# Optimization experiments

Measured on AMD Instinct MI355X. Metric: run time of the kernel, lower is better.

The kernel has to match this reference:

```python
import jax, jax.numpy as jnp
import numpy as np

B, OBS, H, A = 262144, 64, 64, 16
ACTION_LOW, ACTION_HIGH = -1.0, 1.0


def setup_inputs() -> dict:
    key = jax.random.key(0)
    ks = jax.random.split(key, 11)
    s = 0.05
    return {
        "obs": jax.random.normal(ks[0], (B, OBS), dtype=jnp.float32),
        "h0": jax.random.normal(ks[1], (1, B, H), dtype=jnp.float32),
        "c0": jax.random.normal(ks[2], (1, B, H), dtype=jnp.float32),
        "W_in": jax.random.normal(ks[3], (H, OBS), dtype=jnp.float32) * s,
        "b_in": jax.random.normal(ks[4], (H,), dtype=jnp.float32) * s,
        "W_ih": jax.random.normal(ks[5], (4 * H, H), dtype=jnp.float32) * s,
        "W_hh": jax.random.normal(ks[6], (4 * H, H), dtype=jnp.float32) * s,
        "b_ih": jax.random.normal(ks[7], (4 * H,), dtype=jnp.float32) * s,
        "b_hh": jax.random.normal(ks[8], (4 * H,), dtype=jnp.float32) * s,
        "W_out": jax.random.normal(ks[9], (A, H), dtype=jnp.float32) * s,
        "b_out": jax.random.normal(ks[10], (A,), dtype=jnp.float32) * s,
    }


def reference(obs, h0, c0, W_in, b_in, W_ih, W_hh, b_ih, b_hh, W_out, b_out):
    # input projection: [B, H]
    x = obs @ W_in.T + b_in
    h, c = h0[0], c0[0]  # [B, H] each (num_layers=1, seq_len=1)
    # single-step LSTM cell, PyTorch gate order (i, f, g, o)
    gates = x @ W_ih.T + b_ih + h @ W_hh.T + b_hh  # [B, 4H]
    i, f, g, o = jnp.split(gates, 4, axis=-1)
    i = jax.nn.sigmoid(i)
    f = jax.nn.sigmoid(f)
    g = jnp.tanh(g)
    o = jax.nn.sigmoid(o)
    c_new = f * c + i * g
    h_new = o * jnp.tanh(c_new)
    a = jnp.tanh(h_new @ W_out.T + b_out)  # [B, A]
    action = ACTION_LOW + (a + 1.0) * 0.5 * (ACTION_HIGH - ACTION_LOW)
    return action, h_new[None], c_new[None]
```

## Files before the change

### kernel.cpp

```cpp
#include <hip/hip_runtime.h>
#include <hip/hip_bf16.h>

#define BT 262144
#define BLOCK 512
#define NBLOCKS 512
#define NIT 4

typedef __attribute__((ext_vector_type(8))) short short8;
typedef __attribute__((ext_vector_type(4))) float f32x4;
typedef __attribute__((ext_vector_type(4))) unsigned short u16x4;

__device__ __forceinline__ unsigned short f2bf(float f) {
  union { __hip_bfloat16 b; unsigned short u; } v;
  v.b = __float2bfloat16(f);
  return v.u;
}
__device__ __forceinline__ float frcp(float x) { return __builtin_amdgcn_rcpf(x); }
__device__ __forceinline__ float sigm(float x) { return frcp(1.0f + __expf(-x)); }
__device__ __forceinline__ float tanh_(float x) {
  float e = __expf(-2.0f * x);
  return (1.0f - e) * frcp(1.0f + e);
}

__global__ void prep_kernel(const float* __restrict__ W_in, const float* __restrict__ b_in,
                            const float* __restrict__ W_ih, const float* __restrict__ W_hh,
                            const float* __restrict__ b_ih, const float* __restrict__ b_hh,
                            const float* __restrict__ W_out,
                            unsigned short* __restrict__ wsW, float* __restrict__ ws_beff) {
  int id = blockIdx.x * blockDim.x + threadIdx.x;
  if (id < 16384) {
    int j = id & 7, l = (id >> 3) & 63, a = (id >> 9) & 15, ks = id >> 13;
    int n = (a >> 2) * 64 + 4 * (l & 15) + (a & 3);
    int k = ks * 32 + (l >> 4) * 8 + j;
    float s = 0.f;
    #pragma unroll 8
    for (int h = 0; h < 64; ++h) s = fmaf(W_ih[n * 64 + h], W_in[h * 64 + k], s);
    wsW[id] = f2bf(s);
  } else if (id < 32768) {
    int e = id - 16384;
    int j = e & 7, l = (e >> 3) & 63, a = (e >> 9) & 15, ks = (e >> 13) & 1;
    int n = (a >> 2) * 64 + 4 * (l & 15) + (a & 3);
    int k = ks * 32 + (l >> 4) * 8 + j;
    wsW[id] = f2bf(W_hh[n * 64 + k]);
  } else if (id < 33792) {
    int e = id - 32768;
    int j = e & 7, l = (e >> 3) & 63, ks = e >> 9;
    int n = l & 15;
    int k = ks * 32 + (l >> 4) * 8 + j;
    wsW[id] = f2bf(W_out[n * 64 + k]);
  } else if (id < 34048) {
    int n = id - 33792;
    float s = b_ih[n] + b_hh[n];
    #pragma unroll 8
    for (int h = 0; h < 64; ++h) s = fmaf(W_ih[n * 64 + h], b_in[h], s);
    ws_beff[n] = s;
  }
}

__device__ __forceinline__ short8 pack8(float4 lo, float4 hi) {
  short8 r;
  r[0] = (short)f2bf(lo.x); r[1] = (short)f2bf(lo.y);
  r[2] = (short)f2bf(lo.z); r[3] = (short)f2bf(lo.w);
  r[4] = (short)f2bf(hi.x); r[5] = (short)f2bf(hi.y);
  r[6] = (short)f2bf(hi.z); r[7] = (short)f2bf(hi.w);
  return r;
}

__global__ __launch_bounds__(BLOCK, 2) void lstm_main(
    const float* __restrict__ obs, const float* __restrict__ h0,
    const float* __restrict__ c0, const float* __restrict__ b_out,
    const unsigned short* __restrict__ wsW, const float* __restrict__ ws_beff,
    float* __restrict__ out) {
  __shared__ __attribute__((aligned(16))) unsigned char sbuf[65536];
  __shared__ __attribute__((aligned(16))) unsigned short hbuf[8][1024];
  unsigned short* sw = (unsigned short*)sbuf;

  const int tid = threadIdx.x;
  const int wv = tid >> 6;
  const int lane = tid & 63;
  const int l16 = lane & 15;
  const int q = lane >> 4;

  for (int i = tid; i < 4096; i += BLOCK)
    ((uint4*)sbuf)[i] = ((const uint4*)wsW)[i];
  __syncthreads();

  const float boA = b_out[l16];

  const short8* wEv = (const short8*)sw;
  const short8* wHv = (const short8*)(sw + 16384);
  const short8* wOg = (const short8*)(wsW + 32768);
  unsigned short* hb = &hbuf[wv][0];

  float* out_act = out;
  float* out_h = out + (size_t)BT * 16;
  float* out_c = out + (size_t)BT * 80;

  float4 ro[2][4], rh[2][4];
  f32x4 cold[2][4];

  auto tile_rowbase = [&](int it) -> size_t {
    return ((size_t)(it * NBLOCKS + blockIdx.x)) * 128 + (size_t)wv * 16;
  };
  auto load_oh = [&](int it, int buf) {
    size_t rowbase = tile_rowbase(it);
    const float* po = obs + (rowbase + l16) * 64 + q * 8;
    const float* ph = h0 + (rowbase + l16) * 64 + q * 8;
    ro[buf][0] = *(const float4*)(po);
    ro[buf][1] = *(const float4*)(po + 4);
    ro[buf][2] = *(const float4*)(po + 32);
    ro[buf][3] = *(const float4*)(po + 36);
    rh[buf][0] = *(const float4*)(ph);
    rh[buf][1] = *(const float4*)(ph + 4);
    rh[buf][2] = *(const float4*)(ph + 32);
    rh[buf][3] = *(const float4*)(ph + 36);
  };
  auto load_c0 = [&](int it, int buf) {
    size_t rowbase = tile_rowbase(it);
    #pragma unroll
    for (int r = 0; r < 4; ++r)
      cold[buf][r] = *(const f32x4*)(c0 + (rowbase + (size_t)(4 * q + r)) * 64 + 4 * l16);
  };

  load_oh(0, 0);
  load_c0(0, 0);
  #pragma unroll
  for (int it = 0; it < NIT; ++it) {
    const int cur = it & 1;
    const size_t rowbase = tile_rowbase(it);

    if (it + 1 < NIT) {
      load_oh(it + 1, cur ^ 1);
      load_c0(it + 1, cur ^ 1);
    }

    f32x4 bias_g[4];
    #pragma unroll
    for (int g = 0; g < 4; ++g)
      bias_g[g] = *(const f32x4*)(ws_beff + g * 64 + 4 * l16);

    short8 aObs[2], aH[2];
    aObs[0] = pack8(ro[cur][0], ro[cur][1]);
    aObs[1] = pack8(ro[cur][2], ro[cur][3]);
    aH[0]   = pack8(rh[cur][0], rh[cur][1]);
    aH[1]   = pack8(rh[cur][2], rh[cur][3]);

    f32x4 acc[16];
    #pragma unroll
    for (int a = 0; a < 16; ++a) {
      float b = bias_g[a >> 2][a & 3];
      acc[a] = (f32x4){b, b, b, b};
    }

    #pragma unroll
    for (int ks = 0; ks < 2; ++ks) {
      #pragma unroll
      for (int a = 0; a < 16; ++a) {
        acc[a] = __builtin_amdgcn_mfma_f32_16x16x32_bf16(aObs[ks], wEv[(ks * 16 + a) * 64 + lane], acc[a], 0, 0, 0);
        acc[a] = __builtin_amdgcn_mfma_f32_16x16x32_bf16(aH[ks],  wHv[(ks * 16 + a) * 64 + lane], acc[a], 0, 0, 0);
      }
    }

    #pragma unroll
    for (int r = 0; r < 4; ++r) {
      f32x4 c4, h4;
      u16x4 hb4;
      #pragma unroll
      for (int t = 0; t < 4; ++t) {
        float iv = sigm(acc[t][r]);
        float fv = sigm(acc[4 + t][r]);
        float gv = tanh_(acc[8 + t][r]);
        float ov = sigm(acc[12 + t][r]);
        float cnew = fmaf(fv, cold[cur][r][t], iv * gv);
        float hnew = ov * tanh_(cnew);
        c4[t] = cnew;
        h4[t] = hnew;
        hb4[t] = f2bf(hnew);
      }
      const int hrow = 4 * q + r;
      const size_t m = rowbase + (size_t)hrow;
      __builtin_nontemporal_store(c4, (f32x4*)(out_c + m * 64 + 4 * l16));
      __builtin_nontemporal_store(h4, (f32x4*)(out_h + m * 64 + 4 * l16));
      *(u16x4*)(hb + hrow * 64 + ((4 * l16) ^ ((hrow & 7) << 3))) = hb4;
    }

    f32x4 aA = (f32x4){boA, boA, boA, boA};
    short8 a0 = *(const short8*)(hb + l16 * 64 + ((0 * 32 + q * 8) ^ ((l16 & 7) << 3)));
    short8 a1 = *(const short8*)(hb + l16 * 64 + ((1 * 32 + q * 8) ^ ((l16 & 7) << 3)));
    aA = __builtin_amdgcn_mfma_f32_16x16x32_bf16(a0, wOg[lane], aA, 0, 0, 0);
    aA = __builtin_amdgcn_mfma_f32_16x16x32_bf16(a1, wOg[64 + lane], aA, 0, 0, 0);
    #pragma unroll
    for (int r = 0; r < 4; ++r) {
      size_t m = rowbase + (size_t)(4 * q + r);
      __builtin_nontemporal_store(tanh_(aA[r]), out_act + m * 16 + l16);
    }
  }
}

extern "C" void kernel_launch(void* const* d_in, const int* in_sizes, int n_in,
                              void* d_out, int out_size, void* d_ws, size_t ws_size,
                              hipStream_t stream) {
  const float* obs  = (const float*)d_in[0];
  const float* h0   = (const float*)d_in[1];
  const float* c0   = (const float*)d_in[2];
  const float* W_in = (const float*)d_in[3];
  const float* b_in = (const float*)d_in[4];
  const float* W_ih = (const float*)d_in[5];
  const float* W_hh = (const float*)d_in[6];
  const float* b_ih = (const float*)d_in[7];
  const float* b_hh = (const float*)d_in[8];
  const float* W_out = (const float*)d_in[9];
  const float* b_out = (const float*)d_in[10];

  unsigned short* wsW = (unsigned short*)d_ws;
  float* ws_beff = (float*)((char*)d_ws + 67584);

  prep_kernel<<<133, 256, 0, stream>>>(W_in, b_in, W_ih, W_hh, b_ih, b_hh, W_out, wsW, ws_beff);
  lstm_main<<<NBLOCKS, BLOCK, 0, stream>>>(obs, h0, c0, b_out, wsW, ws_beff, (float*)d_out);
}
```

Before: 68.22 us.

## Split output-head projection into a separate kernel reading h from global

Moves the action head (h_new @ W_out + tanh) out of the main LSTM kernel into a new act_kernel that re-reads h_new from the output buffer. This drops the per-wave LDS h buffer and the head MFMAs from the main kernel, freeing LDS and registers for occupancy, and h stores become regular cached stores so the second kernel may hit in cache. In exchange it adds a kernel launch and an extra 64 MB read of h from memory.

```diff
diff --git a/kernel.cpp b/kernel.cpp
--- a/kernel.cpp
+++ b/kernel.cpp
@@ -8,7 +8,6 @@
 
 typedef __attribute__((ext_vector_type(8))) short short8;
 typedef __attribute__((ext_vector_type(4))) float f32x4;
-typedef __attribute__((ext_vector_type(4))) unsigned short u16x4;
 
 __device__ __forceinline__ unsigned short f2bf(float f) {
   union { __hip_bfloat16 b; unsigned short u; } v;
@@ -68,11 +67,10 @@
 
 __global__ __launch_bounds__(BLOCK, 2) void lstm_main(
     const float* __restrict__ obs, const float* __restrict__ h0,
-    const float* __restrict__ c0, const float* __restrict__ b_out,
+    const float* __restrict__ c0,
     const unsigned short* __restrict__ wsW, const float* __restrict__ ws_beff,
     float* __restrict__ out) {
   __shared__ __attribute__((aligned(16))) unsigned char sbuf[65536];
-  __shared__ __attribute__((aligned(16))) unsigned short hbuf[8][1024];
   unsigned short* sw = (unsigned short*)sbuf;
 
   const int tid = threadIdx.x;
@@ -85,14 +83,9 @@
     ((uint4*)sbuf)[i] = ((const uint4*)wsW)[i];
   __syncthreads();
 
-  const float boA = b_out[l16];
-
   const short8* wEv = (const short8*)sw;
   const short8* wHv = (const short8*)(sw + 16384);
-  const short8* wOg = (const short8*)(wsW + 32768);
-  unsigned short* hb = &hbuf[wv][0];
-
-  float* out_act = out;
+
   float* out_h = out + (size_t)BT * 16;
   float* out_c = out + (size_t)BT * 80;
 
@@ -164,7 +157,6 @@
     #pragma unroll
     for (int r = 0; r < 4; ++r) {
       f32x4 c4, h4;
-      u16x4 hb4;
       #pragma unroll
       for (int t = 0; t < 4; ++t) {
         float iv = sigm(acc[t][r]);
@@ -175,25 +167,43 @@
         float hnew = ov * tanh_(cnew);
         c4[t] = cnew;
         h4[t] = hnew;
-        hb4[t] = f2bf(hnew);
       }
       const int hrow = 4 * q + r;
       const size_t m = rowbase + (size_t)hrow;
       __builtin_nontemporal_store(c4, (f32x4*)(out_c + m * 64 + 4 * l16));
-      __builtin_nontemporal_store(h4, (f32x4*)(out_h + m * 64 + 4 * l16));
-      *(u16x4*)(hb + hrow * 64 + ((4 * l16) ^ ((hrow & 7) << 3))) = hb4;
-    }
-
-    f32x4 aA = (f32x4){boA, boA, boA, boA};
-    short8 a0 = *(const short8*)(hb + l16 * 64 + ((0 * 32 + q * 8) ^ ((l16 & 7) << 3)));
-    short8 a1 = *(const short8*)(hb + l16 * 64 + ((1 * 32 + q * 8) ^ ((l16 & 7) << 3)));
-    aA = __builtin_amdgcn_mfma_f32_16x16x32_bf16(a0, wOg[lane], aA, 0, 0, 0);
-    aA = __builtin_amdgcn_mfma_f32_16x16x32_bf16(a1, wOg[64 + lane], aA, 0, 0, 0);
-    #pragma unroll
-    for (int r = 0; r < 4; ++r) {
-      size_t m = rowbase + (size_t)(4 * q + r);
-      __builtin_nontemporal_store(tanh_(aA[r]), out_act + m * 16 + l16);
-    }
+      *(f32x4*)(out_h + m * 64 + 4 * l16) = h4;
+    }
+  }
+}
+
+__global__ void act_kernel(const float* __restrict__ h,
+                           const float* __restrict__ b_out,
+                           const unsigned short* __restrict__ wsW,
+                           float* __restrict__ out_act) {
+  const int tid = threadIdx.x;
+  const int wv = tid >> 6;
+  const int lane = tid & 63;
+  const int l16 = lane & 15;
+  const int q = lane >> 4;
+  const size_t rowbase = ((size_t)blockIdx.x * 4 + (size_t)wv) * 16;
+
+  const float* ph = h + (rowbase + l16) * 64 + q * 8;
+  float4 h0v = *(const float4*)(ph);
+  float4 h1v = *(const float4*)(ph + 4);
+  float4 h2v = *(const float4*)(ph + 32);
+  float4 h3v = *(const float4*)(ph + 36);
+  short8 a0 = pack8(h0v, h1v);
+  short8 a1 = pack8(h2v, h3v);
+
+  const short8* wOg = (const short8*)(wsW + 32768);
+  const float bo = b_out[l16];
+  f32x4 aA = (f32x4){bo, bo, bo, bo};
+  aA = __builtin_amdgcn_mfma_f32_16x16x32_bf16(a0, wOg[lane], aA, 0, 0, 0);
+  aA = __builtin_amdgcn_mfma_f32_16x16x32_bf16(a1, wOg[64 + lane], aA, 0, 0, 0);
+  #pragma unroll
+  for (int r = 0; r < 4; ++r) {
+    size_t m = rowbase + (size_t)(4 * q + r);
+    __builtin_nontemporal_store(tanh_(aA[r]), out_act + m * 16 + l16);
   }
 }
 
@@ -215,6 +225,10 @@
   unsigned short* wsW = (unsigned short*)d_ws;
   float* ws_beff = (float*)((char*)d_ws + 67584);
 
+  float* out = (float*)d_out;
+  float* out_h = out + (size_t)BT * 16;
+
   prep_kernel<<<133, 256, 0, stream>>>(W_in, b_in, W_ih, W_hh, b_ih, b_hh, W_out, wsW, ws_beff);
-  lstm_main<<<NBLOCKS, BLOCK, 0, stream>>>(obs, h0, c0, b_out, wsW, ws_beff, (float*)d_out);
-}
+  lstm_main<<<NBLOCKS, BLOCK, 0, stream>>>(obs, h0, c0, wsW, ws_beff, out);
+  act_kernel<<<BT / 64, 256, 0, stream>>>(out_h, b_out, wsW, out);
+}
```

Result: slower. 84.48 us (+23.8%).

## Shrink blocks to 6 waves, target 3 blocks per CU, stage bias in LDS

Applied to the files above, without the earlier changes.

Reduces the block size to 384 threads (6 waves, 96 rows per tile) and raises launch bounds to 3 blocks per CU, so more waves can be resident and hide memory latency. Iterations grow to 6, with a guard skipping tiles past the batch end. The effective bias moves into shared memory alongside the weights instead of being reloaded from global memory each iteration. The obs/h0 prefetch buffer is single-buffered, with packing done before the next prefetch to cut register use. LDS use per block rises slightly, and the higher occupancy target may force register spills.

```diff
diff --git a/kernel.cpp b/kernel.cpp
--- a/kernel.cpp
+++ b/kernel.cpp
@@ -2,9 +2,10 @@
 #include <hip/hip_bf16.h>
 
 #define BT 262144
-#define BLOCK 512
+#define BLOCK 384
 #define NBLOCKS 512
-#define NIT 4
+#define NIT 6
+#define ROWS_PER_TILE 96
 
 typedef __attribute__((ext_vector_type(8))) short short8;
 typedef __attribute__((ext_vector_type(4))) float f32x4;
@@ -66,13 +67,12 @@
   return r;
 }
 
-__global__ __launch_bounds__(BLOCK, 2) void lstm_main(
+__global__ __launch_bounds__(BLOCK, 3) void lstm_main(
     const float* __restrict__ obs, const float* __restrict__ h0,
     const float* __restrict__ c0, const float* __restrict__ b_out,
-    const unsigned short* __restrict__ wsW, const float* __restrict__ ws_beff,
-    float* __restrict__ out) {
-  __shared__ __attribute__((aligned(16))) unsigned char sbuf[65536];
-  __shared__ __attribute__((aligned(16))) unsigned short hbuf[8][1024];
+    const unsigned short* __restrict__ wsW, float* __restrict__ out) {
+  __shared__ __attribute__((aligned(16))) unsigned char sbuf[66560];
+  __shared__ __attribute__((aligned(16))) unsigned short hbuf[6][1024];
   unsigned short* sw = (unsigned short*)sbuf;
 
   const int tid = threadIdx.x;
@@ -81,74 +81,78 @@
   const int l16 = lane & 15;
   const int q = lane >> 4;
 
-  for (int i = tid; i < 4096; i += BLOCK)
-    ((uint4*)sbuf)[i] = ((const uint4*)wsW)[i];
+  for (int i = tid; i < 4160; i += BLOCK)
+    ((uint4*)sbuf)[i] = ((const uint4*)wsW)[i < 4096 ? i : i + 128];
   __syncthreads();
 
-  const float boA = b_out[l16];
-
+  const float* beff_s = (const float*)(sbuf + 65536);
   const short8* wEv = (const short8*)sw;
   const short8* wHv = (const short8*)(sw + 16384);
   const short8* wOg = (const short8*)(wsW + 32768);
   unsigned short* hb = &hbuf[wv][0];
+  const float boA = b_out[l16];
 
   float* out_act = out;
   float* out_h = out + (size_t)BT * 16;
   float* out_c = out + (size_t)BT * 80;
 
-  float4 ro[2][4], rh[2][4];
+  float4 ro[4], rh[4];
+  short8 aObs[2], aH[2];
   f32x4 cold[2][4];
 
-  auto tile_rowbase = [&](int it) -> size_t {
-    return ((size_t)(it * NBLOCKS + blockIdx.x)) * 128 + (size_t)wv * 16;
+  auto rowstart_of = [&](int it) -> unsigned {
+    return (unsigned)(it * NBLOCKS + blockIdx.x) * ROWS_PER_TILE + (unsigned)wv * 16;
   };
-  auto load_oh = [&](int it, int buf) {
-    size_t rowbase = tile_rowbase(it);
-    const float* po = obs + (rowbase + l16) * 64 + q * 8;
-    const float* ph = h0 + (rowbase + l16) * 64 + q * 8;
-    ro[buf][0] = *(const float4*)(po);
-    ro[buf][1] = *(const float4*)(po + 4);
-    ro[buf][2] = *(const float4*)(po + 32);
-    ro[buf][3] = *(const float4*)(po + 36);
-    rh[buf][0] = *(const float4*)(ph);
-    rh[buf][1] = *(const float4*)(ph + 4);
-    rh[buf][2] = *(const float4*)(ph + 32);
-    rh[buf][3] = *(const float4*)(ph + 36);
+  auto load_oh = [&](unsigned rowstart) {
+    const float* po = obs + (size_t)(rowstart + l16) * 64 + q * 8;
+    const float* ph = h0 + (size_t)(rowstart + l16) * 64 + q * 8;
+    ro[0] = *(const float4*)(po);
+    ro[1] = *(const float4*)(po + 4);
+    ro[2] = *(const float4*)(po + 32);
+    ro[3] = *(const float4*)(po + 36);
+    rh[0] = *(const float4*)(ph);
+    rh[1] = *(const float4*)(ph + 4);
+    rh[2] = *(const float4*)(ph + 32);
+    rh[3] = *(const float4*)(ph + 36);
   };
-  auto load_c0 = [&](int it, int buf) {
-    size_t rowbase = tile_rowbase(it);
+
+  {
+    unsigned rs0 = rowstart_of(0);
+    load_oh(rs0);
     #pragma unroll
     for (int r = 0; r < 4; ++r)
-      cold[buf][r] = *(const f32x4*)(c0 + (rowbase + (size_t)(4 * q + r)) * 64 + 4 * l16);
-  };
-
-  load_oh(0, 0);
-  load_c0(0, 0);
+      cold[0][r] = *(const f32x4*)(c0 + (size_t)(rs0 + 4 * q + r) * 64 + 4 * l16);
+  }
+
   #pragma unroll
   for (int it = 0; it < NIT; ++it) {
     const int cur = it & 1;
-    const size_t rowbase = tile_rowbase(it);
+    const unsigned rowstart = rowstart_of(it);
+    const bool active = rowstart < BT;
+
+    if (active) {
+      aObs[0] = pack8(ro[0], ro[1]);
+      aObs[1] = pack8(ro[2], ro[3]);
+      aH[0]   = pack8(rh[0], rh[1]);
+      aH[1]   = pack8(rh[2], rh[3]);
+    }
 
     if (it + 1 < NIT) {
-      load_oh(it + 1, cur ^ 1);
-      load_c0(it + 1, cur ^ 1);
-    }
-
-    f32x4 bias_g[4];
-    #pragma unroll
-    for (int g = 0; g < 4; ++g)
-      bias_g[g] = *(const f32x4*)(ws_beff + g * 64 + 4 * l16);
-
-    short8 aObs[2], aH[2];
-    aObs[0] = pack8(ro[cur][0], ro[cur][1]);
-    aObs[1] = pack8(ro[cur][2], ro[cur][3]);
-    aH[0]   = pack8(rh[cur][0], rh[cur][1]);
-    aH[1]   = pack8(rh[cur][2], rh[cur][3]);
+      unsigned rs2 = rowstart_of(it + 1);
+      if (rs2 < BT) {
+        load_oh(rs2);
+        #pragma unroll
+        for (int r = 0; r < 4; ++r)
+          cold[cur ^ 1][r] = *(const f32x4*)(c0 + (size_t)(rs2 + 4 * q + r) * 64 + 4 * l16);
+      }
+    }
+
+    if (!active) continue;
 
     f32x4 acc[16];
     #pragma unroll
     for (int a = 0; a < 16; ++a) {
-      float b = bias_g[a >> 2][a & 3];
+      float b = beff_s[(a >> 2) * 64 + 4 * l16 + (a & 3)];
       acc[a] = (f32x4){b, b, b, b};
     }
 
@@ -178,9 +182,9 @@
         hb4[t] = f2bf(hnew);
       }
       const int hrow = 4 * q + r;
-      const size_t m = rowbase + (size_t)hrow;
-      __builtin_nontemporal_store(c4, (f32x4*)(out_c + m * 64 + 4 * l16));
-      __builtin_nontemporal_store(h4, (f32x4*)(out_h + m * 64 + 4 * l16));
+      const unsigned m = rowstart + (unsigned)hrow;
+      __builtin_nontemporal_store(c4, (f32x4*)(out_c + (size_t)m * 64 + 4 * l16));
+      __builtin_nontemporal_store(h4, (f32x4*)(out_h + (size_t)m * 64 + 4 * l16));
       *(u16x4*)(hb + hrow * 64 + ((4 * l16) ^ ((hrow & 7) << 3))) = hb4;
     }
 
@@ -191,8 +195,8 @@
     aA = __builtin_amdgcn_mfma_f32_16x16x32_bf16(a1, wOg[64 + lane], aA, 0, 0, 0);
     #pragma unroll
     for (int r = 0; r < 4; ++r) {
-      size_t m = rowbase + (size_t)(4 * q + r);
-      __builtin_nontemporal_store(tanh_(aA[r]), out_act + m * 16 + l16);
+      unsigned m = rowstart + (unsigned)(4 * q + r);
+      __builtin_nontemporal_store(tanh_(aA[r]), out_act + (size_t)m * 16 + l16);
     }
   }
 }
@@ -216,5 +220,5 @@
   float* ws_beff = (float*)((char*)d_ws + 67584);
 
   prep_kernel<<<133, 256, 0, stream>>>(W_in, b_in, W_ih, W_hh, b_ih, b_hh, W_out, wsW, ws_beff);
-  lstm_main<<<NBLOCKS, BLOCK, 0, stream>>>(obs, h0, c0, b_out, wsW, ws_beff, (float*)d_out);
-}
+  lstm_main<<<NBLOCKS, BLOCK, 0, stream>>>(obs, h0, c0, b_out, wsW, (float*)d_out);
+}
```

Measured after the change: 103.7 us. 1.52x slower.
